# Kernel tuning notes

Hardware: AMD Instinct MI355X
Metric: run time of the kernel (lower is better)

## Reference

```python
import jax, jax.numpy as jnp
import numpy as np

N, E, D, L = 50000, 800000, 128, 4


def setup_inputs() -> dict:
    key = jax.random.key(0)
    k0, k1, k2, k3 = jax.random.split(key, 4)
    x = jax.random.normal(k0, (N, D), dtype=jnp.float32)
    edge_index = jax.random.randint(k1, (2, E), 0, N, dtype=jnp.int32)
    # per-layer GCNConv weights [L, D, D] and biases [L, D]
    W = jax.random.normal(k2, (L, D, D), dtype=jnp.float32) * (1.0 / np.sqrt(D))
    b = jax.random.normal(k3, (L, D), dtype=jnp.float32) * 0.01
    batch_index = jnp.zeros((N,), dtype=jnp.int32)
    node_rankings = jnp.zeros((N,), dtype=jnp.int32)
    return {"x": x, "edge_index": edge_index, "batch_index": batch_index,
            "node_rankings": node_rankings, "W": W, "b": b}


def reference(x, edge_index, batch_index, node_rankings, W, b):
    # NullControl contributes 0; dropout_rate=0 / eval -> identity.
    n = x.shape[0]
    loops = jnp.arange(n, dtype=edge_index.dtype)
    row = jnp.concatenate([edge_index[0], loops])  # sources (with self-loops)
    col = jnp.concatenate([edge_index[1], loops])  # destinations
    # symmetric GCN normalization: deg over destinations, norm = d_i^-1/2 d_j^-1/2
    deg = jax.ops.segment_sum(jnp.ones_like(row, dtype=x.dtype), col, num_segments=n)
    dinv = jnp.where(deg > 0, jax.lax.rsqrt(deg), 0.0)
    norm = dinv[row] * dinv[col]  # [E+N]
    for l in range(W.shape[0]):
        h = x @ W[l]                      # [N, D] dense transform
        msg = h[row] * norm[:, None]      # [E+N, D] gathered, scaled messages
        agg = jax.ops.segment_sum(msg, col, num_segments=n)  # scatter-add
        x = jax.nn.relu(agg + b[l])       # control(=0) + bias + relu
    return x
```

## Files before the change

### kernel.cpp

```cpp
#include <hip/hip_runtime.h>

#define D 128
#define NLAYERS 4

typedef unsigned short ushort_t;
typedef unsigned int uint_t;

__device__ __forceinline__ ushort_t f2bf(float f) {
    uint_t u = __float_as_uint(f);
    u += 0x7FFFu + ((u >> 16) & 1u);
    return (ushort_t)(u >> 16);
}
__device__ __forceinline__ float bf_lo(uint_t u) {
    return __uint_as_float(u << 16);
}
__device__ __forceinline__ float bf_hi(uint_t u) {
    return __uint_as_float(u & 0xFFFF0000u);
}


__global__ void k_count_deg(const int* __restrict__ dsts, int E,
                            int* __restrict__ deg, int* __restrict__ slot) {
    int i = blockIdx.x * blockDim.x + threadIdx.x;
    if (i < E) slot[i] = atomicAdd(&deg[dsts[i]], 1);
}

__global__ void k_scan1(const int* __restrict__ deg, int n, int* __restrict__ out,
                        int* __restrict__ partials, float* __restrict__ dinv) {
    __shared__ int wsum[4];
    int tid = threadIdx.x;
    int base = blockIdx.x * 1024 + tid * 4;
    int d0 = (base + 0 < n) ? deg[base + 0] : 0;
    int d1 = (base + 1 < n) ? deg[base + 1] : 0;
    int d2 = (base + 2 < n) ? deg[base + 2] : 0;
    int d3 = (base + 3 < n) ? deg[base + 3] : 0;
    if (base + 0 < n) dinv[base + 0] = rsqrtf((float)(d0 + 1));
    if (base + 1 < n) dinv[base + 1] = rsqrtf((float)(d1 + 1));
    if (base + 2 < n) dinv[base + 2] = rsqrtf((float)(d2 + 1));
    if (base + 3 < n) dinv[base + 3] = rsqrtf((float)(d3 + 1));
    int s = d0 + d1 + d2 + d3;
    int lane = tid & 63;
    int incl = s;
    #pragma unroll
    for (int off = 1; off < 64; off <<= 1) {
        int y = __shfl_up(incl, off);
        if (lane >= off) incl += y;
    }
    int wid = tid >> 6;
    if (lane == 63) wsum[wid] = incl;
    __syncthreads();
    int wprev = 0;
    for (int w = 0; w < wid; w++) wprev += wsum[w];
    int excl = wprev + (incl - s);
    if (base + 0 < n) out[base + 0] = excl;
    if (base + 1 < n) out[base + 1] = excl + d0;
    if (base + 2 < n) out[base + 2] = excl + d0 + d1;
    if (base + 3 < n) out[base + 3] = excl + d0 + d1 + d2;
    if (tid == 255) partials[blockIdx.x] = wprev + incl;
}

__global__ void k_scan2(int* partials, int nb) {
    if (threadIdx.x == 0 && blockIdx.x == 0) {
        int acc = 0;
        for (int i = 0; i < nb; i++) { int t = partials[i]; partials[i] = acc; acc += t; }
    }
}

__global__ void k_scan3(int* __restrict__ row_ptr, const int* __restrict__ partials,
                        int n, int E) {
    int i = blockIdx.x * blockDim.x + threadIdx.x;
    if (i < n) row_ptr[i] += partials[i >> 10];
    if (i == 0) row_ptr[n] = E;
}

__global__ void k_place(const int* __restrict__ srcs, const int* __restrict__ dsts, int E,
                        const int* __restrict__ row_ptr, const int* __restrict__ slot,
                        const float* __restrict__ dinv, int2* __restrict__ ew) {
    int i = blockIdx.x * blockDim.x + threadIdx.x;
    if (i >= E) return;
    int c = dsts[i], r = srcs[i];
    int pos = row_ptr[c] + slot[i];
    int2 v;
    v.x = r;
    v.y = __float_as_int(dinv[r]);
    ew[pos] = v;
}

__global__ void k_tobf16(const float* __restrict__ x, ushort_t* __restrict__ xh,
                         int total4) {
    int i = blockIdx.x * blockDim.x + threadIdx.x;
    if (i >= total4) return;
    float4 v = ((const float4*)x)[i];
    uint2 o;
    o.x = (uint_t)f2bf(v.x) | ((uint_t)f2bf(v.y) << 16);
    o.y = (uint_t)f2bf(v.z) | ((uint_t)f2bf(v.w) << 16);
    ((uint2*)xh)[i] = o;
}

__global__ __launch_bounds__(256) void k_aggregate(
    const ushort_t* __restrict__ xh, const int* __restrict__ row_ptr,
    const int2* __restrict__ ew, const float* __restrict__ dinv,
    float* __restrict__ s, int n) {
    int gwave = (blockIdx.x * 256 + threadIdx.x) >> 6;
    if (gwave >= n) return;
    int lane = threadIdx.x & 63;
    int sub = lane >> 4;
    int t = lane & 15;
    int node = gwave;
    float di = dinv[node];

    float acc[8];
    {
        uint4 v = *(const uint4*)(xh + (size_t)node * D + t * 8);
        float w = (sub == 0) ? di : 0.f;
        acc[0] = w * bf_lo(v.x); acc[1] = w * bf_hi(v.x);
        acc[2] = w * bf_lo(v.y); acc[3] = w * bf_hi(v.y);
        acc[4] = w * bf_lo(v.z); acc[5] = w * bf_hi(v.z);
        acc[6] = w * bf_lo(v.w); acc[7] = w * bf_hi(v.w);
    }
    int e = row_ptr[node], end = row_ptr[node + 1];
    for (; e + 8 <= end; e += 8) {
        int2 g0 = ew[e + sub];
        int2 g1 = ew[e + 4 + sub];
        uint4 v0 = *(const uint4*)(xh + (size_t)g0.x * D + t * 8);
        uint4 v1 = *(const uint4*)(xh + (size_t)g1.x * D + t * 8);
        float w0 = __int_as_float(g0.y);
        float w1 = __int_as_float(g1.y);
        acc[0] += w0 * bf_lo(v0.x); acc[1] += w0 * bf_hi(v0.x);
        acc[2] += w0 * bf_lo(v0.y); acc[3] += w0 * bf_hi(v0.y);
        acc[4] += w0 * bf_lo(v0.z); acc[5] += w0 * bf_hi(v0.z);
        acc[6] += w0 * bf_lo(v0.w); acc[7] += w0 * bf_hi(v0.w);
        acc[0] += w1 * bf_lo(v1.x); acc[1] += w1 * bf_hi(v1.x);
        acc[2] += w1 * bf_lo(v1.y); acc[3] += w1 * bf_hi(v1.y);
        acc[4] += w1 * bf_lo(v1.z); acc[5] += w1 * bf_hi(v1.z);
        acc[6] += w1 * bf_lo(v1.w); acc[7] += w1 * bf_hi(v1.w);
    }
    for (; e < end; e += 4) {
        int rem = end - e;
        int k = (sub < rem) ? sub : 0;
        int2 g = ew[e + k];
        float w = (sub < rem) ? __int_as_float(g.y) : 0.f;
        uint4 v = *(const uint4*)(xh + (size_t)g.x * D + t * 8);
        acc[0] += w * bf_lo(v.x); acc[1] += w * bf_hi(v.x);
        acc[2] += w * bf_lo(v.y); acc[3] += w * bf_hi(v.y);
        acc[4] += w * bf_lo(v.z); acc[5] += w * bf_hi(v.z);
        acc[6] += w * bf_lo(v.w); acc[7] += w * bf_hi(v.w);
    }
    #pragma unroll
    for (int q = 0; q < 8; q++) {
        acc[q] += __shfl_xor(acc[q], 16);
        acc[q] += __shfl_xor(acc[q], 32);
    }
    if (sub == 0) {
        float* dst = s + (size_t)node * D + t * 8;
        float4 o0, o1;
        o0.x = di * acc[0]; o0.y = di * acc[1]; o0.z = di * acc[2]; o0.w = di * acc[3];
        o1.x = di * acc[4]; o1.y = di * acc[5]; o1.z = di * acc[6]; o1.w = di * acc[7];
        *(float4*)dst = o0;
        *(float4*)(dst + 4) = o1;
    }
}

__global__ __launch_bounds__(256) void k_gemm_bias_relu(
    const float* __restrict__ A, const float* __restrict__ Wl,
    const float* __restrict__ bias, float* __restrict__ out_f32,
    ushort_t* __restrict__ out_bf, int n) {
    __shared__ float As[64][D];
    int tid = threadIdx.x;
    int brow = blockIdx.x * 64;
    #pragma unroll
    for (int p = 0; p < 8; p++) {
        int r = p * 8 + (tid >> 5);
        int c = (tid & 31) * 4;
        int gr = brow + r;
        if (gr > n - 1) gr = n - 1;
        float4 v = *(const float4*)(A + (size_t)gr * D + c);
        *(float4*)&As[r][c] = v;
    }
    __syncthreads();
    int rg = tid >> 5;
    int cg = tid & 31;
    int c0 = cg * 4;
    float acc[8][4];
    #pragma unroll
    for (int j = 0; j < 8; j++)
        #pragma unroll
        for (int q = 0; q < 4; q++) acc[j][q] = 0.f;

    for (int k0 = 0; k0 < D; k0 += 4) {
        float4 w0 = *(const float4*)(Wl + (size_t)(k0 + 0) * D + c0);
        float4 w1 = *(const float4*)(Wl + (size_t)(k0 + 1) * D + c0);
        float4 w2 = *(const float4*)(Wl + (size_t)(k0 + 2) * D + c0);
        float4 w3 = *(const float4*)(Wl + (size_t)(k0 + 3) * D + c0);
        #pragma unroll
        for (int j = 0; j < 8; j++) {
            float4 a = *(const float4*)&As[rg * 8 + j][k0];
            acc[j][0] += a.x * w0.x + a.y * w1.x + a.z * w2.x + a.w * w3.x;
            acc[j][1] += a.x * w0.y + a.y * w1.y + a.z * w2.y + a.w * w3.y;
            acc[j][2] += a.x * w0.z + a.y * w1.z + a.z * w2.z + a.w * w3.z;
            acc[j][3] += a.x * w0.w + a.y * w1.w + a.z * w2.w + a.w * w3.w;
        }
    }
    float4 bv = *(const float4*)(bias + c0);
    #pragma unroll
    for (int j = 0; j < 8; j++) {
        int gr = brow + rg * 8 + j;
        if (gr < n) {
            float o0 = fmaxf(acc[j][0] + bv.x, 0.f);
            float o1 = fmaxf(acc[j][1] + bv.y, 0.f);
            float o2 = fmaxf(acc[j][2] + bv.z, 0.f);
            float o3 = fmaxf(acc[j][3] + bv.w, 0.f);
            if (out_bf) {
                uint2 o;
                o.x = (uint_t)f2bf(o0) | ((uint_t)f2bf(o1) << 16);
                o.y = (uint_t)f2bf(o2) | ((uint_t)f2bf(o3) << 16);
                *(uint2*)(out_bf + (size_t)gr * D + c0) = o;
            } else {
                float4 o;
                o.x = o0; o.y = o1; o.z = o2; o.w = o3;
                *(float4*)(out_f32 + (size_t)gr * D + c0) = o;
            }
        }
    }
}


extern "C" void kernel_launch(void* const* d_in, const int* in_sizes, int n_in,
                              void* d_out, int out_size, void* d_ws, size_t ws_size,
                              hipStream_t stream) {
    const float* x   = (const float*)d_in[0];
    const int* eidx  = (const int*)d_in[1];
    const float* W   = (const float*)d_in[4];
    const float* b   = (const float*)d_in[5];
    float* out       = (float*)d_out;

    const int N = in_sizes[0] / D;
    const int E = in_sizes[1] / 2;
    const int* srcs = eidx;
    const int* dsts = eidx + E;

    char* ws = (char*)d_ws;
    size_t off = 0;
    auto alloc = [&](size_t bytes) -> void* {
        void* p = ws + off;
        off = (off + bytes + 511) & ~(size_t)511;
        return p;
    };
    int*      deg      = (int*)alloc((size_t)N * 4);
    float*    dinv     = (float*)alloc((size_t)N * 4);
    int*      row_ptr  = (int*)alloc((size_t)(N + 1) * 4);
    int*      partials = (int*)alloc(256 * 4);
    int2*     ew       = (int2*)alloc((size_t)E * 8);
    float*    s_buf    = (float*)alloc((size_t)N * D * 4);
    ushort_t* xh0      = (ushort_t*)alloc((size_t)N * D * 2);
    ushort_t* xh1      = (ushort_t*)alloc((size_t)N * D * 2);
    int*      slot     = (int*)s_buf;
    (void)ws_size; (void)n_in; (void)out_size;

    hipMemsetAsync(deg, 0, (size_t)N * 4, stream);

    int tE = (E + 255) / 256;
    int tN = (N + 255) / 256;
    int nbScan = (N + 1023) / 1024;

    k_count_deg<<<tE, 256, 0, stream>>>(dsts, E, deg, slot);
    k_scan1<<<nbScan, 256, 0, stream>>>(deg, N, row_ptr, partials, dinv);
    k_scan2<<<1, 64, 0, stream>>>(partials, nbScan);
    k_scan3<<<tN, 256, 0, stream>>>(row_ptr, partials, N, E);
    k_place<<<tE, 256, 0, stream>>>(srcs, dsts, E, row_ptr, slot, dinv, ew);

    int total4 = N * D / 4;
    k_tobf16<<<(total4 + 255) / 256, 256, 0, stream>>>(x, xh0, total4);

    int aggBlocks = (N + 3) / 4;
    int gemmBlocks = (N + 63) / 64;

    const ushort_t* xin = xh0;
    for (int l = 0; l < NLAYERS; l++) {
        k_aggregate<<<aggBlocks, 256, 0, stream>>>(xin, row_ptr, ew, dinv, s_buf, N);
        bool last = (l == NLAYERS - 1);
        ushort_t* xout = last ? nullptr : ((l & 1) ? xh0 : xh1);
        k_gemm_bias_relu<<<gemmBlocks, 256, 0, stream>>>(
            s_buf, W + (size_t)l * D * D, b + (size_t)l * D,
            last ? out : nullptr, xout, N);
        xin = xout;
    }
}
```

Before: 416.1 us.

## Replace FP32 GEMM with bf16 MFMA using split hi/lo weights

Replaces the scalar FP32 shared-memory GEMM with a matrix-core version built on 16x16x32 bf16 MFMA. Weights are pre-transposed and split into bf16 high and low parts to keep extra precision. The aggregation output is now stored as bf16, which halves the intermediate buffer traffic, and the aggregation inner loop is unrolled to 16 edges to keep more gathers in flight. In exchange, the activations fed to the GEMM are rounded to bf16 and the epilogue writes scalar, non-vectorized stores.

```diff
diff --git a/kernel.cpp b/kernel.cpp
--- a/kernel.cpp
+++ b/kernel.cpp
@@ -5,6 +5,8 @@
 
 typedef unsigned short ushort_t;
 typedef unsigned int uint_t;
+typedef __attribute__((ext_vector_type(8))) short short8;
+typedef __attribute__((ext_vector_type(4))) float f32x4;
 
 __device__ __forceinline__ ushort_t f2bf(float f) {
     uint_t u = __float_as_uint(f);
@@ -16,6 +18,9 @@
 }
 __device__ __forceinline__ float bf_hi(uint_t u) {
     return __uint_as_float(u & 0xFFFF0000u);
+}
+__device__ __forceinline__ uint_t pack2(float a, float b) {
+    return (uint_t)f2bf(a) | ((uint_t)f2bf(b) << 16);
 }
 
 
@@ -86,21 +91,36 @@
     ew[pos] = v;
 }
 
+__global__ void k_wprep(const float* __restrict__ W, ushort_t* __restrict__ Wt_hi,
+                        ushort_t* __restrict__ Wt_lo) {
+    int t = blockIdx.x * 256 + threadIdx.x;
+    int l = t >> 14;
+    int k = (t >> 7) & 127;
+    int nn = t & 127;
+    float w = W[((size_t)l << 14) + k * 128 + nn];
+    ushort_t hi = f2bf(w);
+    float wf = __uint_as_float((uint_t)hi << 16);
+    ushort_t lo = f2bf(w - wf);
+    size_t o = ((size_t)l << 14) + nn * 128 + k;
+    Wt_hi[o] = hi;
+    Wt_lo[o] = lo;
+}
+
 __global__ void k_tobf16(const float* __restrict__ x, ushort_t* __restrict__ xh,
                          int total4) {
     int i = blockIdx.x * blockDim.x + threadIdx.x;
     if (i >= total4) return;
     float4 v = ((const float4*)x)[i];
     uint2 o;
-    o.x = (uint_t)f2bf(v.x) | ((uint_t)f2bf(v.y) << 16);
-    o.y = (uint_t)f2bf(v.z) | ((uint_t)f2bf(v.w) << 16);
+    o.x = pack2(v.x, v.y);
+    o.y = pack2(v.z, v.w);
     ((uint2*)xh)[i] = o;
 }
 
 __global__ __launch_bounds__(256) void k_aggregate(
     const ushort_t* __restrict__ xh, const int* __restrict__ row_ptr,
     const int2* __restrict__ ew, const float* __restrict__ dinv,
-    float* __restrict__ s, int n) {
+    ushort_t* __restrict__ s, int n) {
     int gwave = (blockIdx.x * 256 + threadIdx.x) >> 6;
     if (gwave >= n) return;
     int lane = threadIdx.x & 63;
@@ -119,13 +139,19 @@
         acc[6] = w * bf_lo(v.w); acc[7] = w * bf_hi(v.w);
     }
     int e = row_ptr[node], end = row_ptr[node + 1];
-    for (; e + 8 <= end; e += 8) {
+    for (; e + 16 <= end; e += 16) {
         int2 g0 = ew[e + sub];
         int2 g1 = ew[e + 4 + sub];
+        int2 g2 = ew[e + 8 + sub];
+        int2 g3 = ew[e + 12 + sub];
         uint4 v0 = *(const uint4*)(xh + (size_t)g0.x * D + t * 8);
         uint4 v1 = *(const uint4*)(xh + (size_t)g1.x * D + t * 8);
+        uint4 v2 = *(const uint4*)(xh + (size_t)g2.x * D + t * 8);
+        uint4 v3 = *(const uint4*)(xh + (size_t)g3.x * D + t * 8);
         float w0 = __int_as_float(g0.y);
         float w1 = __int_as_float(g1.y);
+        float w2 = __int_as_float(g2.y);
+        float w3 = __int_as_float(g3.y);
         acc[0] += w0 * bf_lo(v0.x); acc[1] += w0 * bf_hi(v0.x);
         acc[2] += w0 * bf_lo(v0.y); acc[3] += w0 * bf_hi(v0.y);
         acc[4] += w0 * bf_lo(v0.z); acc[5] += w0 * bf_hi(v0.z);
@@ -134,6 +160,14 @@
         acc[2] += w1 * bf_lo(v1.y); acc[3] += w1 * bf_hi(v1.y);
         acc[4] += w1 * bf_lo(v1.z); acc[5] += w1 * bf_hi(v1.z);
         acc[6] += w1 * bf_lo(v1.w); acc[7] += w1 * bf_hi(v1.w);
+        acc[0] += w2 * bf_lo(v2.x); acc[1] += w2 * bf_hi(v2.x);
+        acc[2] += w2 * bf_lo(v2.y); acc[3] += w2 * bf_hi(v2.y);
+        acc[4] += w2 * bf_lo(v2.z); acc[5] += w2 * bf_hi(v2.z);
+        acc[6] += w2 * bf_lo(v2.w); acc[7] += w2 * bf_hi(v2.w);
+        acc[0] += w3 * bf_lo(v3.x); acc[1] += w3 * bf_hi(v3.x);
+        acc[2] += w3 * bf_lo(v3.y); acc[3] += w3 * bf_hi(v3.y);
+        acc[4] += w3 * bf_lo(v3.z); acc[5] += w3 * bf_hi(v3.z);
+        acc[6] += w3 * bf_lo(v3.w); acc[7] += w3 * bf_hi(v3.w);
     }
     for (; e < end; e += 4) {
         int rem = end - e;
@@ -152,73 +186,74 @@
         acc[q] += __shfl_xor(acc[q], 32);
     }
     if (sub == 0) {
-        float* dst = s + (size_t)node * D + t * 8;
-        float4 o0, o1;
-        o0.x = di * acc[0]; o0.y = di * acc[1]; o0.z = di * acc[2]; o0.w = di * acc[3];
-        o1.x = di * acc[4]; o1.y = di * acc[5]; o1.z = di * acc[6]; o1.w = di * acc[7];
-        *(float4*)dst = o0;
-        *(float4*)(dst + 4) = o1;
-    }
-}
-
-__global__ __launch_bounds__(256) void k_gemm_bias_relu(
-    const float* __restrict__ A, const float* __restrict__ Wl,
-    const float* __restrict__ bias, float* __restrict__ out_f32,
-    ushort_t* __restrict__ out_bf, int n) {
-    __shared__ float As[64][D];
+        ushort_t* dst = s + (size_t)node * D + t * 8;
+        uint4 o;
+        o.x = pack2(di * acc[0], di * acc[1]);
+        o.y = pack2(di * acc[2], di * acc[3]);
+        o.z = pack2(di * acc[4], di * acc[5]);
+        o.w = pack2(di * acc[6], di * acc[7]);
+        *(uint4*)dst = o;
+    }
+}
+
+__global__ __launch_bounds__(256) void k_gemm_mfma(
+    const ushort_t* __restrict__ A, const ushort_t* __restrict__ Wt_hi,
+    const ushort_t* __restrict__ Wt_lo, const float* __restrict__ bias,
+    float* __restrict__ out_f32, ushort_t* __restrict__ out_bf, int n) {
     int tid = threadIdx.x;
-    int brow = blockIdx.x * 64;
-    #pragma unroll
-    for (int p = 0; p < 8; p++) {
-        int r = p * 8 + (tid >> 5);
-        int c = (tid & 31) * 4;
-        int gr = brow + r;
-        if (gr > n - 1) gr = n - 1;
-        float4 v = *(const float4*)(A + (size_t)gr * D + c);
-        *(float4*)&As[r][c] = v;
-    }
-    __syncthreads();
-    int rg = tid >> 5;
-    int cg = tid & 31;
-    int c0 = cg * 4;
-    float acc[8][4];
-    #pragma unroll
-    for (int j = 0; j < 8; j++)
+    int wave = tid >> 6;
+    int lane = tid & 63;
+    int lg = lane >> 4;
+    int lr = lane & 15;
+    int base_row = blockIdx.x * 128 + wave * 32;
+
+    short8 a[2][4];
+    #pragma unroll
+    for (int st = 0; st < 2; st++) {
+        int r = base_row + st * 16 + lr;
+        if (r > n - 1) r = n - 1;
+        const ushort_t* ap = A + (size_t)r * D + lg * 8;
         #pragma unroll
-        for (int q = 0; q < 4; q++) acc[j][q] = 0.f;
-
-    for (int k0 = 0; k0 < D; k0 += 4) {
-        float4 w0 = *(const float4*)(Wl + (size_t)(k0 + 0) * D + c0);
-        float4 w1 = *(const float4*)(Wl + (size_t)(k0 + 1) * D + c0);
-        float4 w2 = *(const float4*)(Wl + (size_t)(k0 + 2) * D + c0);
-        float4 w3 = *(const float4*)(Wl + (size_t)(k0 + 3) * D + c0);
+        for (int k0 = 0; k0 < 4; k0++)
+            a[st][k0] = *(const short8*)(ap + k0 * 32);
+    }
+
+    f32x4 acc[2][8];
+    #pragma unroll
+    for (int st = 0; st < 2; st++)
         #pragma unroll
-        for (int j = 0; j < 8; j++) {
-            float4 a = *(const float4*)&As[rg * 8 + j][k0];
-            acc[j][0] += a.x * w0.x + a.y * w1.x + a.z * w2.x + a.w * w3.x;
-            acc[j][1] += a.x * w0.y + a.y * w1.y + a.z * w2.y + a.w * w3.y;
-            acc[j][2] += a.x * w0.z + a.y * w1.z + a.z * w2.z + a.w * w3.z;
-            acc[j][3] += a.x * w0.w + a.y * w1.w + a.z * w2.w + a.w * w3.w;
+        for (int nt = 0; nt < 8; nt++)
+            acc[st][nt] = (f32x4){0.f, 0.f, 0.f, 0.f};
+
+    #pragma unroll
+    for (int nt = 0; nt < 8; nt++) {
+        const ushort_t* wh = Wt_hi + (size_t)(nt * 16 + lr) * D + lg * 8;
+        const ushort_t* wl = Wt_lo + (size_t)(nt * 16 + lr) * D + lg * 8;
+        #pragma unroll
+        for (int k0 = 0; k0 < 4; k0++) {
+            short8 bh = *(const short8*)(wh + k0 * 32);
+            short8 bl = *(const short8*)(wl + k0 * 32);
+            acc[0][nt] = __builtin_amdgcn_mfma_f32_16x16x32_bf16(a[0][k0], bh, acc[0][nt], 0, 0, 0);
+            acc[0][nt] = __builtin_amdgcn_mfma_f32_16x16x32_bf16(a[0][k0], bl, acc[0][nt], 0, 0, 0);
+            acc[1][nt] = __builtin_amdgcn_mfma_f32_16x16x32_bf16(a[1][k0], bh, acc[1][nt], 0, 0, 0);
+            acc[1][nt] = __builtin_amdgcn_mfma_f32_16x16x32_bf16(a[1][k0], bl, acc[1][nt], 0, 0, 0);
         }
     }
-    float4 bv = *(const float4*)(bias + c0);
-    #pragma unroll
-    for (int j = 0; j < 8; j++) {
-        int gr = brow + rg * 8 + j;
-        if (gr < n) {
-            float o0 = fmaxf(acc[j][0] + bv.x, 0.f);
-            float o1 = fmaxf(acc[j][1] + bv.y, 0.f);
-            float o2 = fmaxf(acc[j][2] + bv.z, 0.f);
-            float o3 = fmaxf(acc[j][3] + bv.w, 0.f);
-            if (out_bf) {
-                uint2 o;
-                o.x = (uint_t)f2bf(o0) | ((uint_t)f2bf(o1) << 16);
-                o.y = (uint_t)f2bf(o2) | ((uint_t)f2bf(o3) << 16);
-                *(uint2*)(out_bf + (size_t)gr * D + c0) = o;
-            } else {
-                float4 o;
-                o.x = o0; o.y = o1; o.z = o2; o.w = o3;
-                *(float4*)(out_f32 + (size_t)gr * D + c0) = o;
+
+    #pragma unroll
+    for (int nt = 0; nt < 8; nt++) {
+        int col = nt * 16 + lr;
+        float bv = bias[col];
+        #pragma unroll
+        for (int st = 0; st < 2; st++) {
+            #pragma unroll
+            for (int r = 0; r < 4; r++) {
+                int grow = base_row + st * 16 + lg * 4 + r;
+                if (grow < n) {
+                    float o = fmaxf(acc[st][nt][r] + bv, 0.f);
+                    if (out_bf) out_bf[(size_t)grow * D + col] = f2bf(o);
+                    else out_f32[(size_t)grow * D + col] = o;
+                }
             }
         }
     }
@@ -251,9 +286,11 @@
     int*      row_ptr  = (int*)alloc((size_t)(N + 1) * 4);
     int*      partials = (int*)alloc(256 * 4);
     int2*     ew       = (int2*)alloc((size_t)E * 8);
-    float*    s_buf    = (float*)alloc((size_t)N * D * 4);
+    ushort_t* s_buf    = (ushort_t*)alloc((size_t)N * D * 2);
     ushort_t* xh0      = (ushort_t*)alloc((size_t)N * D * 2);
     ushort_t* xh1      = (ushort_t*)alloc((size_t)N * D * 2);
+    ushort_t* wt_hi    = (ushort_t*)alloc((size_t)NLAYERS * D * D * 2);
+    ushort_t* wt_lo    = (ushort_t*)alloc((size_t)NLAYERS * D * D * 2);
     int*      slot     = (int*)s_buf;
     (void)ws_size; (void)n_in; (void)out_size;
 
@@ -268,21 +305,22 @@
     k_scan2<<<1, 64, 0, stream>>>(partials, nbScan);
     k_scan3<<<tN, 256, 0, stream>>>(row_ptr, partials, N, E);
     k_place<<<tE, 256, 0, stream>>>(srcs, dsts, E, row_ptr, slot, dinv, ew);
+    k_wprep<<<(NLAYERS * D * D) / 256, 256, 0, stream>>>(W, wt_hi, wt_lo);
 
     int total4 = N * D / 4;
     k_tobf16<<<(total4 + 255) / 256, 256, 0, stream>>>(x, xh0, total4);
 
     int aggBlocks = (N + 3) / 4;
-    int gemmBlocks = (N + 63) / 64;
+    int gemmBlocks = (N + 127) / 128;
 
     const ushort_t* xin = xh0;
     for (int l = 0; l < NLAYERS; l++) {
         k_aggregate<<<aggBlocks, 256, 0, stream>>>(xin, row_ptr, ew, dinv, s_buf, N);
         bool last = (l == NLAYERS - 1);
         ushort_t* xout = last ? nullptr : ((l & 1) ? xh0 : xh1);
-        k_gemm_bias_relu<<<gemmBlocks, 256, 0, stream>>>(
-            s_buf, W + (size_t)l * D * D, b + (size_t)l * D,
-            last ? out : nullptr, xout, N);
+        k_gemm_mfma<<<gemmBlocks, 256, 0, stream>>>(
+            s_buf, wt_hi + (size_t)l * D * D, wt_lo + (size_t)l * D * D,
+            b + (size_t)l * D, last ? out : nullptr, xout, N);
         xin = xout;
     }
 }
```

Measured after the change: 387.2 us. -6.9%, faster.
